# Performance work log

Hardware: AMD Instinct MI355X
Metric: run time of the kernel (lower is better)

Reference implementation:

```python
import jax, jax.numpy as jnp
import numpy as np

BATCH, SEQLEN, DMODEL, DSTATE = 8, 2048, 1024, 16


def setup_inputs() -> dict:
    key = jax.random.key(0)
    ks = jax.random.split(key, 6)
    u = jax.random.normal(ks[0], (BATCH, SEQLEN, DMODEL), dtype=jnp.float32)
    # delta (discretization step) is positive in Mamba (post-softplus); sample small positive values
    delta = jax.random.uniform(ks[1], (BATCH, SEQLEN, DMODEL), dtype=jnp.float32, minval=0.001, maxval=0.1)
    # A must be negative so exp(delta*A) is a decay in (0,1)
    A = -jnp.exp(jax.random.normal(ks[2], (DMODEL, DSTATE), dtype=jnp.float32) * 0.5)
    B_mat = jax.random.normal(ks[3], (BATCH, SEQLEN, DSTATE), dtype=jnp.float32)
    C_mat = jax.random.normal(ks[4], (BATCH, SEQLEN, DSTATE), dtype=jnp.float32)
    D_vec = jax.random.normal(ks[5], (DMODEL,), dtype=jnp.float32)
    return {"u": u, "delta": delta, "A": A, "B_mat": B_mat, "C_mat": C_mat, "D_vec": D_vec}


def reference(u, delta, A, B_mat, C_mat, D_vec):
    """Selective scan (Mamba-style):
       h_t = exp(delta_t * A) * h_{t-1} + (delta_t * u_t) * B_t
       y_t = <h_t, C_t> + D * u_t
    u, delta: [B, L, D]; A: [D, N]; B_mat, C_mat: [B, L, N]; D_vec: [D].
    """
    def scan_fn(h, xs):
        u_t, d_t, b_t, c_t = xs                      # [B,D],[B,D],[B,N],[B,N]
        dA = jnp.exp(d_t[..., None] * A)             # [B,D,N] decay
        dBu = (d_t * u_t)[..., None] * b_t[:, None, :]  # [B,D,N] driven input
        h = dA * h + dBu                             # [B,D,N]
        y = jnp.einsum('bdn,bn->bd', h, c_t)         # [B,D]
        return h, y

    h0 = jnp.zeros((u.shape[0], u.shape[2], A.shape[1]), dtype=u.dtype)
    # time-leading layout for lax.scan
    xs = (jnp.swapaxes(u, 0, 1), jnp.swapaxes(delta, 0, 1),
          jnp.swapaxes(B_mat, 0, 1), jnp.swapaxes(C_mat, 0, 1))
    _, ys = jax.lax.scan(scan_fn, h0, xs)            # ys: [L,B,D]
    y = jnp.swapaxes(ys, 0, 1) + u * D_vec           # [B,L,D]
    return y
```

## Files before the change

### kernel.cpp

```cpp
#include <hip/hip_runtime.h>

#define BATCH   8
#define SEQLEN  2048
#define DMODEL  1024
#define DSTATE  16
#define BLOCK   256
#define LOG2E   1.4426950408889634f

template<int NC>
__global__ __launch_bounds__(BLOCK) void ssm_phaseA(
    const float* __restrict__ u,  const float* __restrict__ de,
    const float* __restrict__ A,  const float* __restrict__ Bm,
    float* __restrict__ ws_h, float* __restrict__ ws_d)
{
    constexpr int TC = SEQLEN / NC;
    __shared__ float sB[TC * DSTATE];
    const int tid = threadIdx.x;
    const int d   = blockIdx.x * BLOCK + tid;
    const int c   = blockIdx.y;
    const int b   = blockIdx.z;
    const int t0  = c * TC;

    {
        const float4* src = (const float4*)(Bm + (size_t)(b * SEQLEN + t0) * DSTATE);
        float4* dst = (float4*)sB;
        for (int i = tid; i < TC * DSTATE / 4; i += BLOCK)
            dst[i] = src[i];
    }
    __syncthreads();

    float A2[DSTATE];
    #pragma unroll
    for (int n = 0; n < DSTATE; n += 4) {
        float4 a4 = *(const float4*)(A + (size_t)d * DSTATE + n);
        A2[n+0] = a4.x * LOG2E; A2[n+1] = a4.y * LOG2E;
        A2[n+2] = a4.z * LOG2E; A2[n+3] = a4.w * LOG2E;
    }
    float h[DSTATE];
    #pragma unroll
    for (int n = 0; n < DSTATE; ++n) h[n] = 0.f;
    float dsum = 0.f;

    const float* up = u  + (size_t)(b * SEQLEN + t0) * DMODEL + d;
    const float* dp = de + (size_t)(b * SEQLEN + t0) * DMODEL + d;

    #pragma unroll 2
    for (int t = 0; t < TC; ++t) {
        float dl = dp[(size_t)t * DMODEL];
        float uu = up[(size_t)t * DMODEL];
        dsum += dl;
        float du = dl * uu;
        #pragma unroll
        for (int n = 0; n < DSTATE; n += 4) {
            float4 b4 = *(const float4*)(sB + t * DSTATE + n);
            h[n+0] = __builtin_amdgcn_exp2f(dl * A2[n+0]) * h[n+0] + du * b4.x;
            h[n+1] = __builtin_amdgcn_exp2f(dl * A2[n+1]) * h[n+1] + du * b4.y;
            h[n+2] = __builtin_amdgcn_exp2f(dl * A2[n+2]) * h[n+2] + du * b4.z;
            h[n+3] = __builtin_amdgcn_exp2f(dl * A2[n+3]) * h[n+3] + du * b4.w;
        }
    }

    float* wh = ws_h + (size_t)(b * NC + c) * DSTATE * DMODEL + d;
    #pragma unroll
    for (int n = 0; n < DSTATE; ++n) wh[(size_t)n * DMODEL] = h[n];
    ws_d[(size_t)(b * NC + c) * DMODEL + d] = dsum;
}

template<int NC>
__global__ __launch_bounds__(BLOCK) void ssm_phaseB(
    const float* __restrict__ A,
    float* __restrict__ ws_h, const float* __restrict__ ws_d)
{
    const int gid = blockIdx.x * BLOCK + threadIdx.x;
    const int d  = gid % DMODEL;
    const int bn = gid / DMODEL;
    const int n  = bn % DSTATE;
    const int b  = bn / DSTATE;

    const float a2 = A[(size_t)d * DSTATE + n] * LOG2E;
    float h = 0.f;
    size_t ih = (size_t)b * NC * DSTATE * DMODEL + (size_t)n * DMODEL + d;
    size_t id = (size_t)b * NC * DMODEL + d;

    #pragma unroll 4
    for (int c = 0; c < NC; ++c) {
        float hl = ws_h[ih];
        float ds = ws_d[id];
        ws_h[ih] = h;
        h = __builtin_amdgcn_exp2f(a2 * ds) * h + hl;
        ih += (size_t)DSTATE * DMODEL;
        id += DMODEL;
    }
}

template<int NC>
__global__ __launch_bounds__(BLOCK) void ssm_phaseC(
    const float* __restrict__ u,  const float* __restrict__ de,
    const float* __restrict__ A,  const float* __restrict__ Bm,
    const float* __restrict__ Cm, const float* __restrict__ Dv,
    const float* __restrict__ ws_h, float* __restrict__ y)
{
    constexpr int TC = SEQLEN / NC;
    __shared__ float sB[TC * DSTATE];
    __shared__ float sC[TC * DSTATE];
    const int tid = threadIdx.x;
    const int d   = blockIdx.x * BLOCK + tid;
    const int c   = blockIdx.y;
    const int b   = blockIdx.z;
    const int t0  = c * TC;

    {
        const float4* srcB = (const float4*)(Bm + (size_t)(b * SEQLEN + t0) * DSTATE);
        const float4* srcC = (const float4*)(Cm + (size_t)(b * SEQLEN + t0) * DSTATE);
        float4* dstB = (float4*)sB;
        float4* dstC = (float4*)sC;
        for (int i = tid; i < TC * DSTATE / 4; i += BLOCK) {
            dstB[i] = srcB[i];
            dstC[i] = srcC[i];
        }
    }
    __syncthreads();

    float A2[DSTATE];
    #pragma unroll
    for (int n = 0; n < DSTATE; n += 4) {
        float4 a4 = *(const float4*)(A + (size_t)d * DSTATE + n);
        A2[n+0] = a4.x * LOG2E; A2[n+1] = a4.y * LOG2E;
        A2[n+2] = a4.z * LOG2E; A2[n+3] = a4.w * LOG2E;
    }

    float h[DSTATE];
    {
        const float* wh = ws_h + (size_t)(b * NC + c) * DSTATE * DMODEL + d;
        #pragma unroll
        for (int n = 0; n < DSTATE; ++n) h[n] = wh[(size_t)n * DMODEL];
    }

    const float Dd = Dv[d];
    const float* up = u  + (size_t)(b * SEQLEN + t0) * DMODEL + d;
    const float* dp = de + (size_t)(b * SEQLEN + t0) * DMODEL + d;
    float* yp = y + (size_t)(b * SEQLEN + t0) * DMODEL + d;

    #pragma unroll 2
    for (int t = 0; t < TC; ++t) {
        float dl = dp[(size_t)t * DMODEL];
        float uu = up[(size_t)t * DMODEL];
        float du  = dl * uu;
        float acc = Dd * uu;
        #pragma unroll
        for (int n = 0; n < DSTATE; n += 4) {
            float4 b4 = *(const float4*)(sB + t * DSTATE + n);
            float4 c4 = *(const float4*)(sC + t * DSTATE + n);
            h[n+0] = __builtin_amdgcn_exp2f(dl * A2[n+0]) * h[n+0] + du * b4.x;
            h[n+1] = __builtin_amdgcn_exp2f(dl * A2[n+1]) * h[n+1] + du * b4.y;
            h[n+2] = __builtin_amdgcn_exp2f(dl * A2[n+2]) * h[n+2] + du * b4.z;
            h[n+3] = __builtin_amdgcn_exp2f(dl * A2[n+3]) * h[n+3] + du * b4.w;
            acc += h[n+0] * c4.x;
            acc += h[n+1] * c4.y;
            acc += h[n+2] * c4.z;
            acc += h[n+3] * c4.w;
        }
        yp[(size_t)t * DMODEL] = acc;
    }
}

__global__ __launch_bounds__(BLOCK) void ssm_naive(
    const float* __restrict__ u,  const float* __restrict__ de,
    const float* __restrict__ A,  const float* __restrict__ Bm,
    const float* __restrict__ Cm, const float* __restrict__ Dv,
    float* __restrict__ y)
{
    const int tid = threadIdx.x;
    const int d   = blockIdx.x * BLOCK + tid;
    const int b   = blockIdx.z;

    float A2[DSTATE];
    #pragma unroll
    for (int n = 0; n < DSTATE; n += 4) {
        float4 a4 = *(const float4*)(A + (size_t)d * DSTATE + n);
        A2[n+0] = a4.x * LOG2E; A2[n+1] = a4.y * LOG2E;
        A2[n+2] = a4.z * LOG2E; A2[n+3] = a4.w * LOG2E;
    }
    float h[DSTATE];
    #pragma unroll
    for (int n = 0; n < DSTATE; ++n) h[n] = 0.f;
    const float Dd = Dv[d];

    const float* up = u  + (size_t)b * SEQLEN * DMODEL + d;
    const float* dp = de + (size_t)b * SEQLEN * DMODEL + d;
    float* yp = y + (size_t)b * SEQLEN * DMODEL + d;

    for (int t = 0; t < SEQLEN; ++t) {
        float dl = dp[(size_t)t * DMODEL];
        float uu = up[(size_t)t * DMODEL];
        float du  = dl * uu;
        float acc = Dd * uu;
        const float* bp = Bm + (size_t)(b * SEQLEN + t) * DSTATE;
        const float* cp = Cm + (size_t)(b * SEQLEN + t) * DSTATE;
        #pragma unroll
        for (int n = 0; n < DSTATE; n += 4) {
            float4 b4 = *(const float4*)(bp + n);
            float4 c4 = *(const float4*)(cp + n);
            h[n+0] = __builtin_amdgcn_exp2f(dl * A2[n+0]) * h[n+0] + du * b4.x;
            h[n+1] = __builtin_amdgcn_exp2f(dl * A2[n+1]) * h[n+1] + du * b4.y;
            h[n+2] = __builtin_amdgcn_exp2f(dl * A2[n+2]) * h[n+2] + du * b4.z;
            h[n+3] = __builtin_amdgcn_exp2f(dl * A2[n+3]) * h[n+3] + du * b4.w;
            acc += h[n+0] * c4.x;
            acc += h[n+1] * c4.y;
            acc += h[n+2] * c4.z;
            acc += h[n+3] * c4.w;
        }
        yp[(size_t)t * DMODEL] = acc;
    }
}

template<int NC>
static void launch_chunked(const float* u, const float* de, const float* A,
                           const float* Bm, const float* Cm, const float* Dv,
                           float* ws_h, float* ws_d, float* y, hipStream_t stream) {
    dim3 grid(DMODEL / BLOCK, NC, BATCH);
    ssm_phaseA<NC><<<grid, BLOCK, 0, stream>>>(u, de, A, Bm, ws_h, ws_d);
    dim3 gridB((BATCH * DSTATE * DMODEL) / BLOCK, 1, 1);
    ssm_phaseB<NC><<<gridB, BLOCK, 0, stream>>>(A, ws_h, ws_d);
    ssm_phaseC<NC><<<grid, BLOCK, 0, stream>>>(u, de, A, Bm, Cm, Dv, ws_h, y);
}

extern "C" void kernel_launch(void* const* d_in, const int* in_sizes, int n_in,
                              void* d_out, int out_size, void* d_ws, size_t ws_size,
                              hipStream_t stream) {
    const float* u  = (const float*)d_in[0];
    const float* de = (const float*)d_in[1];
    const float* A  = (const float*)d_in[2];
    const float* Bm = (const float*)d_in[3];
    const float* Cm = (const float*)d_in[4];
    const float* Dv = (const float*)d_in[5];
    float* y = (float*)d_out;

    auto need = [](int nc) {
        return ((size_t)BATCH * nc * DSTATE * DMODEL +
                (size_t)BATCH * nc * DMODEL) * sizeof(float);
    };

    if (ws_size >= need(64)) {
        float* ws_h = (float*)d_ws;
        float* ws_d = ws_h + (size_t)BATCH * 64 * DSTATE * DMODEL;
        launch_chunked<64>(u, de, A, Bm, Cm, Dv, ws_h, ws_d, y, stream);
    } else if (ws_size >= need(16)) {
        float* ws_h = (float*)d_ws;
        float* ws_d = ws_h + (size_t)BATCH * 16 * DSTATE * DMODEL;
        launch_chunked<16>(u, de, A, Bm, Cm, Dv, ws_h, ws_d, y, stream);
    } else {
        dim3 grid(DMODEL / BLOCK, 1, BATCH);
        ssm_naive<<<grid, BLOCK, 0, stream>>>(u, de, A, Bm, Cm, Dv, y);
    }
}
```

Measured before the change: 116.4 us.

## Process two channels per thread with float2 loads and prefetch next timestep

Phase A and phase C now have each thread handle two adjacent d channels. This lets u, delta and y move as float2 and lets each shared-memory B/C read serve two channels. The next timestep's u and delta are also prefetched, so global load latency overlaps with the exp/FMA work. The price is half as many blocks and threads in the grid, which lowers parallelism and occupancy, plus roughly double the registers per thread.

New measurement: 114.3 us. Within noise of the previous version (-1.8%).

```diff
diff --git a/kernel.cpp b/kernel.cpp
--- a/kernel.cpp
+++ b/kernel.cpp
@@ -5,6 +5,7 @@
 #define DMODEL  1024
 #define DSTATE  16
 #define BLOCK   256
+#define COLS    2
 #define LOG2E   1.4426950408889634f
 
 template<int NC>
@@ -16,7 +17,7 @@
     constexpr int TC = SEQLEN / NC;
     __shared__ float sB[TC * DSTATE];
     const int tid = threadIdx.x;
-    const int d   = blockIdx.x * BLOCK + tid;
+    const int d0  = (blockIdx.x * BLOCK + tid) * COLS;
     const int c   = blockIdx.y;
     const int b   = blockIdx.z;
     const int t0  = c * TC;
@@ -29,41 +30,54 @@
     }
     __syncthreads();
 
-    float A2[DSTATE];
-    #pragma unroll
-    for (int n = 0; n < DSTATE; n += 4) {
-        float4 a4 = *(const float4*)(A + (size_t)d * DSTATE + n);
-        A2[n+0] = a4.x * LOG2E; A2[n+1] = a4.y * LOG2E;
-        A2[n+2] = a4.z * LOG2E; A2[n+3] = a4.w * LOG2E;
-    }
-    float h[DSTATE];
-    #pragma unroll
-    for (int n = 0; n < DSTATE; ++n) h[n] = 0.f;
-    float dsum = 0.f;
-
-    const float* up = u  + (size_t)(b * SEQLEN + t0) * DMODEL + d;
-    const float* dp = de + (size_t)(b * SEQLEN + t0) * DMODEL + d;
-
+    float A2[COLS][DSTATE];
+    #pragma unroll
+    for (int i = 0; i < COLS; ++i)
+        #pragma unroll
+        for (int n = 0; n < DSTATE; n += 4) {
+            float4 a4 = *(const float4*)(A + (size_t)(d0 + i) * DSTATE + n);
+            A2[i][n+0] = a4.x * LOG2E; A2[i][n+1] = a4.y * LOG2E;
+            A2[i][n+2] = a4.z * LOG2E; A2[i][n+3] = a4.w * LOG2E;
+        }
+
+    float h[COLS][DSTATE];
+    #pragma unroll
+    for (int i = 0; i < COLS; ++i)
+        #pragma unroll
+        for (int n = 0; n < DSTATE; ++n) h[i][n] = 0.f;
+    float dsum[COLS] = {0.f, 0.f};
+
+    const float2* up = (const float2*)(u  + (size_t)(b * SEQLEN + t0) * DMODEL + d0);
+    const float2* dp = (const float2*)(de + (size_t)(b * SEQLEN + t0) * DMODEL + d0);
+    constexpr int STRIDE2 = DMODEL / 2;
+
+    float2 uc = up[0], dc = dp[0];
     #pragma unroll 2
     for (int t = 0; t < TC; ++t) {
-        float dl = dp[(size_t)t * DMODEL];
-        float uu = up[(size_t)t * DMODEL];
-        dsum += dl;
-        float du = dl * uu;
+        float2 un, dn;
+        if (t + 1 < TC) { un = up[(size_t)(t+1) * STRIDE2]; dn = dp[(size_t)(t+1) * STRIDE2]; }
+        const float dl[COLS] = {dc.x, dc.y};
+        const float du[COLS] = {dc.x * uc.x, dc.y * uc.y};
+        dsum[0] += dc.x; dsum[1] += dc.y;
         #pragma unroll
         for (int n = 0; n < DSTATE; n += 4) {
             float4 b4 = *(const float4*)(sB + t * DSTATE + n);
-            h[n+0] = __builtin_amdgcn_exp2f(dl * A2[n+0]) * h[n+0] + du * b4.x;
-            h[n+1] = __builtin_amdgcn_exp2f(dl * A2[n+1]) * h[n+1] + du * b4.y;
-            h[n+2] = __builtin_amdgcn_exp2f(dl * A2[n+2]) * h[n+2] + du * b4.z;
-            h[n+3] = __builtin_amdgcn_exp2f(dl * A2[n+3]) * h[n+3] + du * b4.w;
-        }
-    }
-
-    float* wh = ws_h + (size_t)(b * NC + c) * DSTATE * DMODEL + d;
-    #pragma unroll
-    for (int n = 0; n < DSTATE; ++n) wh[(size_t)n * DMODEL] = h[n];
-    ws_d[(size_t)(b * NC + c) * DMODEL + d] = dsum;
+            #pragma unroll
+            for (int i = 0; i < COLS; ++i) {
+                h[i][n+0] = __builtin_amdgcn_exp2f(dl[i] * A2[i][n+0]) * h[i][n+0] + du[i] * b4.x;
+                h[i][n+1] = __builtin_amdgcn_exp2f(dl[i] * A2[i][n+1]) * h[i][n+1] + du[i] * b4.y;
+                h[i][n+2] = __builtin_amdgcn_exp2f(dl[i] * A2[i][n+2]) * h[i][n+2] + du[i] * b4.z;
+                h[i][n+3] = __builtin_amdgcn_exp2f(dl[i] * A2[i][n+3]) * h[i][n+3] + du[i] * b4.w;
+            }
+        }
+        uc = un; dc = dn;
+    }
+
+    float* wh = ws_h + (size_t)(b * NC + c) * DSTATE * DMODEL + d0;
+    #pragma unroll
+    for (int n = 0; n < DSTATE; ++n)
+        *(float2*)(wh + (size_t)n * DMODEL) = make_float2(h[0][n], h[1][n]);
+    *(float2*)(ws_d + (size_t)(b * NC + c) * DMODEL + d0) = make_float2(dsum[0], dsum[1]);
 }
 
 template<int NC>
@@ -104,7 +118,7 @@
     __shared__ float sB[TC * DSTATE];
     __shared__ float sC[TC * DSTATE];
     const int tid = threadIdx.x;
-    const int d   = blockIdx.x * BLOCK + tid;
+    const int d0  = (blockIdx.x * BLOCK + tid) * COLS;
     const int c   = blockIdx.y;
     const int b   = blockIdx.z;
     const int t0  = c * TC;
@@ -121,46 +135,58 @@
     }
     __syncthreads();
 
-    float A2[DSTATE];
-    #pragma unroll
-    for (int n = 0; n < DSTATE; n += 4) {
-        float4 a4 = *(const float4*)(A + (size_t)d * DSTATE + n);
-        A2[n+0] = a4.x * LOG2E; A2[n+1] = a4.y * LOG2E;
-        A2[n+2] = a4.z * LOG2E; A2[n+3] = a4.w * LOG2E;
-    }
-
-    float h[DSTATE];
+    float A2[COLS][DSTATE];
+    #pragma unroll
+    for (int i = 0; i < COLS; ++i)
+        #pragma unroll
+        for (int n = 0; n < DSTATE; n += 4) {
+            float4 a4 = *(const float4*)(A + (size_t)(d0 + i) * DSTATE + n);
+            A2[i][n+0] = a4.x * LOG2E; A2[i][n+1] = a4.y * LOG2E;
+            A2[i][n+2] = a4.z * LOG2E; A2[i][n+3] = a4.w * LOG2E;
+        }
+
+    float h[COLS][DSTATE];
     {
-        const float* wh = ws_h + (size_t)(b * NC + c) * DSTATE * DMODEL + d;
-        #pragma unroll
-        for (int n = 0; n < DSTATE; ++n) h[n] = wh[(size_t)n * DMODEL];
-    }
-
-    const float Dd = Dv[d];
-    const float* up = u  + (size_t)(b * SEQLEN + t0) * DMODEL + d;
-    const float* dp = de + (size_t)(b * SEQLEN + t0) * DMODEL + d;
-    float* yp = y + (size_t)(b * SEQLEN + t0) * DMODEL + d;
-
+        const float* wh = ws_h + (size_t)(b * NC + c) * DSTATE * DMODEL + d0;
+        #pragma unroll
+        for (int n = 0; n < DSTATE; ++n) {
+            float2 hv = *(const float2*)(wh + (size_t)n * DMODEL);
+            h[0][n] = hv.x; h[1][n] = hv.y;
+        }
+    }
+
+    const float2 Dd = *(const float2*)(Dv + d0);
+    const float2* up = (const float2*)(u  + (size_t)(b * SEQLEN + t0) * DMODEL + d0);
+    const float2* dp = (const float2*)(de + (size_t)(b * SEQLEN + t0) * DMODEL + d0);
+    float2* yp = (float2*)(y + (size_t)(b * SEQLEN + t0) * DMODEL + d0);
+    constexpr int STRIDE2 = DMODEL / 2;
+
+    float2 uc = up[0], dc = dp[0];
     #pragma unroll 2
     for (int t = 0; t < TC; ++t) {
-        float dl = dp[(size_t)t * DMODEL];
-        float uu = up[(size_t)t * DMODEL];
-        float du  = dl * uu;
-        float acc = Dd * uu;
+        float2 un, dn;
+        if (t + 1 < TC) { un = up[(size_t)(t+1) * STRIDE2]; dn = dp[(size_t)(t+1) * STRIDE2]; }
+        const float dl[COLS] = {dc.x, dc.y};
+        const float du[COLS] = {dc.x * uc.x, dc.y * uc.y};
+        float acc[COLS] = {Dd.x * uc.x, Dd.y * uc.y};
         #pragma unroll
         for (int n = 0; n < DSTATE; n += 4) {
             float4 b4 = *(const float4*)(sB + t * DSTATE + n);
             float4 c4 = *(const float4*)(sC + t * DSTATE + n);
-            h[n+0] = __builtin_amdgcn_exp2f(dl * A2[n+0]) * h[n+0] + du * b4.x;
-            h[n+1] = __builtin_amdgcn_exp2f(dl * A2[n+1]) * h[n+1] + du * b4.y;
-            h[n+2] = __builtin_amdgcn_exp2f(dl * A2[n+2]) * h[n+2] + du * b4.z;
-            h[n+3] = __builtin_amdgcn_exp2f(dl * A2[n+3]) * h[n+3] + du * b4.w;
-            acc += h[n+0] * c4.x;
-            acc += h[n+1] * c4.y;
-            acc += h[n+2] * c4.z;
-            acc += h[n+3] * c4.w;
-        }
-        yp[(size_t)t * DMODEL] = acc;
+            #pragma unroll
+            for (int i = 0; i < COLS; ++i) {
+                h[i][n+0] = __builtin_amdgcn_exp2f(dl[i] * A2[i][n+0]) * h[i][n+0] + du[i] * b4.x;
+                h[i][n+1] = __builtin_amdgcn_exp2f(dl[i] * A2[i][n+1]) * h[i][n+1] + du[i] * b4.y;
+                h[i][n+2] = __builtin_amdgcn_exp2f(dl[i] * A2[i][n+2]) * h[i][n+2] + du[i] * b4.z;
+                h[i][n+3] = __builtin_amdgcn_exp2f(dl[i] * A2[i][n+3]) * h[i][n+3] + du[i] * b4.w;
+                acc[i] += h[i][n+0] * c4.x;
+                acc[i] += h[i][n+1] * c4.y;
+                acc[i] += h[i][n+2] * c4.z;
+                acc[i] += h[i][n+3] * c4.w;
+            }
+        }
+        yp[(size_t)t * STRIDE2] = make_float2(acc[0], acc[1]);
+        uc = un; dc = dn;
     }
 }
 
@@ -218,7 +244,7 @@
 static void launch_chunked(const float* u, const float* de, const float* A,
                            const float* Bm, const float* Cm, const float* Dv,
                            float* ws_h, float* ws_d, float* y, hipStream_t stream) {
-    dim3 grid(DMODEL / BLOCK, NC, BATCH);
+    dim3 grid(DMODEL / (BLOCK * COLS), NC, BATCH);
     ssm_phaseA<NC><<<grid, BLOCK, 0, stream>>>(u, de, A, Bm, ws_h, ws_d);
     dim3 gridB((BATCH * DSTATE * DMODEL) / BLOCK, 1, 1);
     ssm_phaseB<NC><<<gridB, BLOCK, 0, stream>>>(A, ws_h, ws_d);
```
